# Kernel tuning notes

Measured on AMD Instinct MI355X. Metric: run time of the kernel, lower is better.

The kernel has to match this reference:

```python
import jax, jax.numpy as jnp
import numpy as np


def setup_inputs() -> dict:
    key = jax.random.key(0)
    ks = jax.random.split(key, 10)
    B, C, D, H, W = 2, 512, 8, 32, 32
    Ck = C // 4  # shared KV head dim (and fixed query dim per intended MQA math)
    s = 0.02
    return {
        "x": jax.random.normal(ks[0], (B, C, D, H, W), dtype=jnp.float32),
        "Wq": jax.random.normal(ks[1], (Ck, C), dtype=jnp.float32) * s,
        "bq": jnp.zeros((Ck,), dtype=jnp.float32),
        "Wk": jax.random.normal(ks[2], (Ck, C), dtype=jnp.float32) * s,
        "bk": jnp.zeros((Ck,), dtype=jnp.float32),
        "Wv": jax.random.normal(ks[3], (Ck, C), dtype=jnp.float32) * s,
        "bv": jnp.zeros((Ck,), dtype=jnp.float32),
        "Wo": jax.random.normal(ks[4], (C, C), dtype=jnp.float32) * s,
        "bo": jnp.zeros((C,), dtype=jnp.float32),
    }


def reference(x, Wq, bq, Wk, bk, Wv, bv, Wo, bo):
    B, C, D, H, W = x.shape
    N = D * H * W
    Ck = Wk.shape[0]  # C // 4
    xf = x.reshape(B, C, N)  # flatten spatial dims -> sequence axis
    # 1x1 Conv3d == per-voxel linear projection over channels
    q = jnp.einsum('oc,bcn->bno', Wq, xf) + bq  # [B, N, Ck]
    k = jnp.einsum('oc,bcn->bno', Wk, xf) + bk  # [B, N, Ck]
    v = jnp.einsum('oc,bcn->bno', Wv, xf) + bv  # [B, N, Ck]
    scale = jnp.asarray(Ck, x.dtype) ** -0.5
    attn = jax.nn.softmax(jnp.einsum('bnc,bmc->bnm', q, k) * scale, axis=-1)  # [B, N, N]
    out = jnp.einsum('bnm,bmc->bnc', attn, v)  # [B, N, Ck]
    out = jnp.tile(out, (1, 1, 4))  # repeat(1,1,4) -> [B, N, C]
    out = jnp.einsum('oc,bnc->bon', Wo, out) + bo[None, :, None]  # [B, C, N]
    return out.reshape(B, C, D, H, W) + x
```

## Files before the change

### kernel.cpp

```cpp
#include <hip/hip_runtime.h>
#include <hip/hip_bf16.h>

typedef __bf16 bf16;
typedef __bf16 bf16x8 __attribute__((ext_vector_type(8)));
typedef __bf16 bf16x4 __attribute__((ext_vector_type(4)));
typedef float  f32x4  __attribute__((ext_vector_type(4)));
typedef float  f32x16 __attribute__((ext_vector_type(16)));
typedef unsigned int u32;
typedef u32 u32x4 __attribute__((ext_vector_type(4)));

constexpr int BB = 2, C = 512, NN = 8192, CK = 128;

__device__ __forceinline__ u32 cvt_pk_bf16(float lo, float hi) {
    u32 r;
    asm("v_cvt_pk_bf16_f32 %0, %1, %2" : "=v"(r) : "v"(lo), "v"(hi));
    return r;
}
__device__ __forceinline__ void pl32_swap(u32& a, u32& b) {
    asm("v_permlane32_swap_b32 %0, %1" : "+v"(a), "+v"(b));
}

__global__ __launch_bounds__(256) void k_qkv(
    const float* __restrict__ x,
    const float* __restrict__ Wq, const float* __restrict__ bq,
    const float* __restrict__ Wk, const float* __restrict__ bk,
    const float* __restrict__ Wv, const float* __restrict__ bv,
    bf16* __restrict__ qkv_ws)
{
    const int t = threadIdx.x;
    const int lane = t & 63, w = t >> 6;
    const int lr = lane & 15, lg = lane >> 4;
    const int n0 = blockIdx.x * 128;
    const int which = blockIdx.y;
    const int b = blockIdx.z;
    const float* W    = which == 0 ? Wq : (which == 1 ? Wk : Wv);
    const float* bias = which == 0 ? bq : (which == 1 ? bk : bv);
    bf16* out = qkv_ws + (size_t)which * BB * NN * CK;

    __shared__ __align__(16) char s_xT[128 * 144];
    __shared__ __align__(16) char s_w [128 * 144];

    f32x4 acc[2][8];
#pragma unroll
    for (int m = 0; m < 2; m++)
#pragma unroll
        for (int j = 0; j < 8; j++) acc[m][j] = (f32x4){0.f, 0.f, 0.f, 0.f};

    const float* xb = x + (size_t)b * C * NN;

    const int tok4 = (t & 31) * 4;
    const int c8   = (t >> 5) * 8;
    const int ob   = t >> 2;
    const int c16  = (t & 3) * 16;

    for (int kt = 0; kt < C; kt += 64) {
        __syncthreads();
        {
            float4 v[8];
#pragma unroll
            for (int i = 0; i < 8; i++)
                v[i] = *(const float4*)(xb + (size_t)(kt + c8 + i) * NN + n0 + tok4);
#pragma unroll
            for (int j = 0; j < 4; j++) {
                int tok = tok4 + j;
                bf16x8 pk = { (bf16)v[0].x, (bf16)v[1].x, (bf16)v[2].x, (bf16)v[3].x,
                              (bf16)v[4].x, (bf16)v[5].x, (bf16)v[6].x, (bf16)v[7].x };
                if (j == 1) pk = (bf16x8){ (bf16)v[0].y, (bf16)v[1].y, (bf16)v[2].y, (bf16)v[3].y,
                                           (bf16)v[4].y, (bf16)v[5].y, (bf16)v[6].y, (bf16)v[7].y };
                if (j == 2) pk = (bf16x8){ (bf16)v[0].z, (bf16)v[1].z, (bf16)v[2].z, (bf16)v[3].z,
                                           (bf16)v[4].z, (bf16)v[5].z, (bf16)v[6].z, (bf16)v[7].z };
                if (j == 3) pk = (bf16x8){ (bf16)v[0].w, (bf16)v[1].w, (bf16)v[2].w, (bf16)v[3].w,
                                           (bf16)v[4].w, (bf16)v[5].w, (bf16)v[6].w, (bf16)v[7].w };
                int off = tok * 144 + ((c8 * 2) ^ ((((tok >> 2) & 7)) << 4));
                *(bf16x8*)(s_xT + off) = pk;
            }
        }
#pragma unroll
        for (int p = 0; p < 2; p++) {
            int o = ob + p * 64;
            const float* wp = W + (size_t)o * C + kt + c16;
            float4 a0 = *(const float4*)(wp);
            float4 a1 = *(const float4*)(wp + 4);
            float4 a2 = *(const float4*)(wp + 8);
            float4 a3 = *(const float4*)(wp + 12);
            bf16x8 p0 = { (bf16)a0.x, (bf16)a0.y, (bf16)a0.z, (bf16)a0.w,
                          (bf16)a1.x, (bf16)a1.y, (bf16)a1.z, (bf16)a1.w };
            bf16x8 p1 = { (bf16)a2.x, (bf16)a2.y, (bf16)a2.z, (bf16)a2.w,
                          (bf16)a3.x, (bf16)a3.y, (bf16)a3.z, (bf16)a3.w };
            int perm = ((o >> 2) & 7) << 4;
            *(bf16x8*)(s_w + o * 144 + ((c16 * 2) ^ perm)) = p0;
            *(bf16x8*)(s_w + o * 144 + ((c16 * 2 + 16) ^ perm)) = p1;
        }
        __syncthreads();
#pragma unroll
        for (int ks = 0; ks < 2; ks++) {
            bf16x8 af[2];
#pragma unroll
            for (int m = 0; m < 2; m++) {
                int row = w * 32 + m * 16 + lr;
                af[m] = *(const bf16x8*)(s_xT + row * 144 + ((ks * 64 + lg * 16) ^ ((((row >> 2) & 7)) << 4)));
            }
#pragma unroll
            for (int j = 0; j < 8; j++) {
                int row = j * 16 + lr;
                bf16x8 bfr = *(const bf16x8*)(s_w + row * 144 + ((ks * 64 + lg * 16) ^ ((((row >> 2) & 7)) << 4)));
                acc[0][j] = __builtin_amdgcn_mfma_f32_16x16x32_bf16(af[0], bfr, acc[0][j], 0, 0, 0);
                acc[1][j] = __builtin_amdgcn_mfma_f32_16x16x32_bf16(af[1], bfr, acc[1][j], 0, 0, 0);
            }
        }
    }
#pragma unroll
    for (int m = 0; m < 2; m++)
#pragma unroll
        for (int j = 0; j < 8; j++) {
            int o = j * 16 + lr;
            float bia = bias[o];
#pragma unroll
            for (int r = 0; r < 4; r++) {
                int tok = n0 + w * 32 + m * 16 + lg * 4 + r;
                out[((size_t)b * NN + tok) * CK + o] = (bf16)(acc[m][j][r] + bia);
            }
        }
}

__global__ __launch_bounds__(512, 2) void k_attn(
    const bf16* __restrict__ qkv_ws,
    float* __restrict__ Opart, float* __restrict__ Mw, float* __restrict__ Lw,
    int nsplit)
{
    const int t = threadIdx.x;
    const int lane = t & 63, w = t >> 6;
    const int lq = lane & 31, hi = lane >> 5;

    const int total = 32 * BB * nsplit;
    const int chunkv = total >> 3;
    const int lin = blockIdx.x;
    const int rid = (lin & 7) * chunkv + (lin >> 3);
    const int qt = rid & 31;
    const int bs = rid >> 5;
    const int b = bs & 1, split = bs >> 1;

    const int q0 = qt * 256;
    const int kbeg = split * (NN / nsplit);
    const int nt = (NN / nsplit) / 64;

    const bf16* kg = qkv_ws + (size_t)BB * NN * CK;
    const bf16* vg = qkv_ws + (size_t)2 * BB * NN * CK;

    __shared__ __align__(16) char s_k[2][64 * 256];
    __shared__ __align__(16) char s_vt[2][128 * 128];

    const int kb0 = lq * 256 + ((((lq & 7) ^ hi)) << 4);
    int vbs[4];
#pragma unroll
    for (int db = 0; db < 4; db++) {
        int d = db * 32 + lq;
        vbs[db] = d * 128 + (((((d ^ (d >> 3)) & 7) ^ hi)) << 4);
    }
    const int t2 = t & 255;
    const int sc = t2 & 15, sr = t2 >> 4;
    const int kw_base = (sr * 256 + sc * 16) ^ ((sr & 7) << 4);
    const int vw_base = (sc * 1024 + sr * 8) ^ ((sc & 7) << 4);

    bf16x8 qf[8];
    {
        const float qs = 0.08838834764831845f * 1.4426950408889634f;
        const bf16* qp = qkv_ws + ((size_t)b * NN + q0 + w * 32 + lq) * CK + hi * 8;
#pragma unroll
        for (int ks = 0; ks < 8; ks++) {
            bf16x8 v = *(const bf16x8*)(qp + ks * 16);
#pragma unroll
            for (int i = 0; i < 8; i++) qf[ks][i] = (bf16)((float)v[i] * qs);
        }
    }

    f32x16 oacc[4];
#pragma unroll
    for (int db = 0; db < 4; db++)
#pragma unroll
        for (int i = 0; i < 16; i++) oacc[db][i] = 0.f;
    float mrun = 0.f, lrun = 0.f;

    const bf16* kp = kg + ((size_t)b * NN + kbeg + sr) * CK + sc * 8;
    const bf16* vp = vg + ((size_t)b * NN + kbeg + sr * 4) * CK + sc * 8;
    bf16x8 stg[4];

    auto issue_loads = [&]() {
        if (w < 4) {
#pragma unroll
            for (int p = 0; p < 4; p++) stg[p] = *(const bf16x8*)(kp + (size_t)(16 * p) * CK);
        } else {
#pragma unroll
            for (int p = 0; p < 4; p++) stg[p] = *(const bf16x8*)(vp + (size_t)p * CK);
        }
        kp += (size_t)64 * CK;
        vp += (size_t)64 * CK;
    };

    issue_loads();

    for (int it = 0; it < nt; it++) {
        const int buf = it & 1;
        if (w < 4) {
            char* skw = s_k[buf] + kw_base;
#pragma unroll
            for (int p = 0; p < 4; p++)
                *(bf16x8*)(skw + p * 4096) = stg[p];
        } else {
            char* svw = s_vt[buf];
#pragma unroll
            for (int i = 0; i < 8; i++) {
                bf16x4 pk = { stg[0][i], stg[1][i], stg[2][i], stg[3][i] };
                *(bf16x4*)(svw + (vw_base ^ (i * 144))) = pk;
            }
        }
        __syncthreads();
        if (it + 1 < nt) issue_loads();

        const char* sk = s_k[buf];
        const char* sv = s_vt[buf];

        f32x16 sa0, sa1;
#pragma unroll
        for (int i = 0; i < 16; i++) { sa0[i] = 0.f; sa1[i] = 0.f; }
        __builtin_amdgcn_s_setprio(1);
#pragma unroll
        for (int ks = 0; ks < 8; ks++) {
            bf16x8 kf0 = *(const bf16x8*)(sk + (kb0 ^ (ks * 32)));
            bf16x8 kf1 = *(const bf16x8*)(sk + ((kb0 ^ (ks * 32)) + 8192));
            sa0 = __builtin_amdgcn_mfma_f32_32x32x16_bf16(kf0, qf[ks], sa0, 0, 0, 0);
            sa1 = __builtin_amdgcn_mfma_f32_32x32x16_bf16(kf1, qf[ks], sa1, 0, 0, 0);
        }
        __builtin_amdgcn_s_setprio(0);

        float m8[8];
#pragma unroll
        for (int i = 0; i < 8; i++) m8[i] = fmaxf(sa0[i], sa0[i + 8]);
#pragma unroll
        for (int i = 0; i < 8; i++) m8[i] = fmaxf(m8[i], fmaxf(sa1[i], sa1[i + 8]));
        float pmax = fmaxf(fmaxf(fmaxf(m8[0], m8[1]), fmaxf(m8[2], m8[3])),
                           fmaxf(fmaxf(m8[4], m8[5]), fmaxf(m8[6], m8[7])));
        pmax = fmaxf(pmax, __shfl_xor(pmax, 32));
        bool ok = (pmax <= mrun + 8.f);
        if (!__all(ok)) {
            float mnew = fmaxf(mrun, pmax);
            float corr = exp2f(mrun - mnew);
            mrun = mnew;
            lrun *= corr;
#pragma unroll
            for (int r = 0; r < 16; r++) {
                int qrow = (r & 3) + 8 * (r >> 2) + 4 * hi;
                float co = __shfl(corr, qrow);
#pragma unroll
                for (int db = 0; db < 4; db++) oacc[db][r] *= co;
            }
        }

        f32x16 p0, p1;
#pragma unroll
        for (int i = 0; i < 16; i++) { p0[i] = exp2f(sa0[i] - mrun); p1[i] = exp2f(sa1[i] - mrun); }
        {
            float s0 = ((p0[0] + p0[1]) + (p0[2] + p0[3])) + ((p0[4] + p0[5]) + (p0[6] + p0[7]));
            float s1 = ((p0[8] + p0[9]) + (p0[10] + p0[11])) + ((p0[12] + p0[13]) + (p0[14] + p0[15]));
            float s2 = ((p1[0] + p1[1]) + (p1[2] + p1[3])) + ((p1[4] + p1[5]) + (p1[6] + p1[7]));
            float s3 = ((p1[8] + p1[9]) + (p1[10] + p1[11])) + ((p1[12] + p1[13]) + (p1[14] + p1[15]));
            lrun += (s0 + s1) + (s2 + s3);
        }
        u32 W0[8], W1[8];
#pragma unroll
        for (int j = 0; j < 8; j++) {
            W0[j] = cvt_pk_bf16(p0[2 * j], p0[2 * j + 1]);
            W1[j] = cvt_pk_bf16(p1[2 * j], p1[2 * j + 1]);
        }
        pl32_swap(W0[0], W0[2]); pl32_swap(W0[1], W0[3]);
        pl32_swap(W0[4], W0[6]); pl32_swap(W0[5], W0[7]);
        pl32_swap(W1[0], W1[2]); pl32_swap(W1[1], W1[3]);
        pl32_swap(W1[4], W1[6]); pl32_swap(W1[5], W1[7]);

        __builtin_amdgcn_s_setprio(1);
#pragma unroll
        for (int s = 0; s < 4; s++) {
            u32x4 fw;
            if (s == 0)      fw = (u32x4){W0[0], W0[1], W0[2], W0[3]};
            else if (s == 1) fw = (u32x4){W0[4], W0[5], W0[6], W0[7]};
            else if (s == 2) fw = (u32x4){W1[0], W1[1], W1[2], W1[3]};
            else             fw = (u32x4){W1[4], W1[5], W1[6], W1[7]};
            bf16x8 pa = __builtin_bit_cast(bf16x8, fw);
            const int coff = (s >> 1) * 64 + (s & 1) * 32;
#pragma unroll
            for (int db = 0; db < 4; db++) {
                bf16x8 vf = *(const bf16x8*)(sv + (vbs[db] ^ coff));
                oacc[db] = __builtin_amdgcn_mfma_f32_32x32x16_bf16(pa, vf, oacc[db], 0, 0, 0);
            }
        }
        __builtin_amdgcn_s_setprio(0);
    }

    size_t obase = (((size_t)split * BB + b) * NN + q0 + w * 32);
    float ls = lrun + __shfl_xor(lrun, 32);
    if (lane < 32) {
        Mw[obase + lq] = mrun;
        Lw[obase + lq] = ls;
    }
#pragma unroll
    for (int r = 0; r < 16; r++) {
        int qrow = (r & 3) + 8 * (r >> 2) + 4 * hi;
        float* op = Opart + (obase + qrow) * CK + lq;
#pragma unroll
        for (int db = 0; db < 4; db++) op[db * 32] = oacc[db][r];
    }
}

__global__ __launch_bounds__(256) void k_combine(
    const float* __restrict__ Opart, const float* __restrict__ Mw,
    const float* __restrict__ Lw, bf16* __restrict__ ao, int nsplit)
{
    const int t = threadIdx.x;
    const int b = blockIdx.y;
    const int r0 = blockIdx.x * 64;
    const int d4 = (t & 31) * 4;
#pragma unroll
    for (int p = 0; p < 8; p++) {
        int row = r0 + (t >> 5) + p * 8;
        size_t rbase = (size_t)b * NN + row;
        float M = -1e30f;
        for (int s = 0; s < nsplit; s++)
            M = fmaxf(M, Mw[((size_t)s * BB) * NN + rbase]);
        float L = 0.f;
        float4 acc = {0.f, 0.f, 0.f, 0.f};
        for (int s = 0; s < nsplit; s++) {
            size_t sb = ((size_t)s * BB) * NN + rbase;
            float wgt = exp2f(Mw[sb] - M);
            L += Lw[sb] * wgt;
            float4 v = *(const float4*)(Opart + sb * CK + d4);
            acc.x += v.x * wgt; acc.y += v.y * wgt;
            acc.z += v.z * wgt; acc.w += v.w * wgt;
        }
        float inv = 1.f / L;
        bf16x4 o4 = { (bf16)(acc.x * inv), (bf16)(acc.y * inv),
                      (bf16)(acc.z * inv), (bf16)(acc.w * inv) };
        *(bf16x4*)(ao + rbase * CK + d4) = o4;
    }
}

__global__ __launch_bounds__(256) void k_out(
    const float* __restrict__ x, const float* __restrict__ Wo, const float* __restrict__ bo,
    const bf16* __restrict__ ao, float* __restrict__ y)
{
    const int t = threadIdx.x;
    const int lane = t & 63, w = t >> 6;
    const int lr = lane & 15, lg = lane >> 4;
    const int n0 = blockIdx.x * 128;
    const int o0 = blockIdx.y * 64;
    const int b = blockIdx.z;

    __shared__ __align__(16) char s_w[64 * 256];
    __shared__ __align__(16) char s_a[128 * 256];

    {
        int c4 = (t & 31) * 4, rbase = t >> 5;
#pragma unroll
        for (int p = 0; p < 8; p++) {
            int row = rbase + p * 8;
            const float* wp = Wo + (size_t)(o0 + row) * C + c4;
            float4 a0 = *(const float4*)(wp);
            float4 a1 = *(const float4*)(wp + 128);
            float4 a2 = *(const float4*)(wp + 256);
            float4 a3 = *(const float4*)(wp + 384);
            bf16x4 r4 = { (bf16)(a0.x + a1.x + a2.x + a3.x), (bf16)(a0.y + a1.y + a2.y + a3.y),
                          (bf16)(a0.z + a1.z + a2.z + a3.z), (bf16)(a0.w + a1.w + a2.w + a3.w) };
            int off = (row * 256 + c4 * 2) ^ ((row & 7) << 4);
            *(bf16x4*)(s_w + off) = r4;
        }
    }
    {
        int chunk = t & 15, rbase = t >> 4;
#pragma unroll
        for (int p = 0; p < 8; p++) {
            int row = rbase + p * 16;
            bf16x8 v = *(const bf16x8*)(ao + ((size_t)b * NN + n0 + row) * CK + chunk * 8);
            int off = (row * 256 + chunk * 16) ^ ((row & 7) << 4);
            *(bf16x8*)(s_a + off) = v;
        }
    }
    __syncthreads();

    f32x4 acc[8];
#pragma unroll
    for (int j = 0; j < 8; j++) acc[j] = (f32x4){0.f, 0.f, 0.f, 0.f};
#pragma unroll
    for (int ks = 0; ks < 4; ks++) {
        int row = w * 16 + lr;
        int aoff = (row * 256 + (ks * 32 + lg * 8) * 2) ^ ((row & 7) << 4);
        bf16x8 wf = *(const bf16x8*)(s_w + aoff);
#pragma unroll
        for (int j = 0; j < 8; j++) {
            int nrow = j * 16 + lr;
            int boff = (nrow * 256 + (ks * 32 + lg * 8) * 2) ^ ((nrow & 7) << 4);
            bf16x8 af = *(const bf16x8*)(s_a + boff);
            acc[j] = __builtin_amdgcn_mfma_f32_16x16x32_bf16(wf, af, acc[j], 0, 0, 0);
        }
    }
#pragma unroll
    for (int j = 0; j < 8; j++) {
        int n = n0 + j * 16 + lr;
#pragma unroll
        for (int r = 0; r < 4; r++) {
            int o = o0 + w * 16 + lg * 4 + r;
            size_t idx = ((size_t)b * C + o) * NN + n;
            y[idx] = acc[j][r] + bo[o] + x[idx];
        }
    }
}

extern "C" void kernel_launch(void* const* d_in, const int* in_sizes, int n_in,
                              void* d_out, int out_size, void* d_ws, size_t ws_size,
                              hipStream_t stream)
{
    const float* x  = (const float*)d_in[0];
    const float* Wq = (const float*)d_in[1];
    const float* bq = (const float*)d_in[2];
    const float* Wk = (const float*)d_in[3];
    const float* bk = (const float*)d_in[4];
    const float* Wv = (const float*)d_in[5];
    const float* bv = (const float*)d_in[6];
    const float* Wo = (const float*)d_in[7];
    const float* bo = (const float*)d_in[8];
    float* y = (float*)d_out;

    const size_t qkv_elems = (size_t)3 * BB * NN * CK;
    const size_t ao_elems  = (size_t)BB * NN * CK;

    bf16* qkv = (bf16*)d_ws;
    bf16* ao  = qkv + qkv_elems;
    float* Opart = (float*)(ao + ao_elems);

    int nsplit = 4;
    {
        size_t fixed = (qkv_elems + ao_elems) * sizeof(bf16);
        size_t per_split = ((size_t)BB * NN * CK + 2 * (size_t)BB * NN) * sizeof(float);
        while (nsplit > 1 && fixed + (size_t)nsplit * per_split > ws_size) nsplit >>= 1;
    }
    float* Mw = Opart + (size_t)nsplit * BB * NN * CK;
    float* Lw = Mw + (size_t)nsplit * BB * NN;

    k_qkv<<<dim3(NN / 128, 3, BB), 256, 0, stream>>>(x, Wq, bq, Wk, bk, Wv, bv, qkv);
    k_attn<<<dim3(32 * BB * nsplit, 1, 1), 512, 0, stream>>>(qkv, Opart, Mw, Lw, nsplit);
    k_combine<<<dim3(NN / 64, BB), 256, 0, stream>>>(Opart, Mw, Lw, ao, nsplit);
    k_out<<<dim3(NN / 128, C / 64, BB), 256, 0, stream>>>(x, Wo, bo, ao, y);
}
```

Measured before the change: 155.4 us.

## Process two query tiles per wave in attention to reuse K/V fragments

The attention kernel now uses 256 threads per block, and each wave handles 64 query rows as two 32-row halves that share every K and V fragment read from LDS. This halves LDS fragment reads per MFMA. The score tile is also processed in two 32-key halves, each with its own online-softmax update. Every thread now loads both K and V staging data, which roughly doubles register pressure (two accumulator sets and two Q fragment sets), and launch bounds drop to one block per CU, lowering occupancy.

```diff
diff --git a/kernel.cpp b/kernel.cpp
--- a/kernel.cpp
+++ b/kernel.cpp
@@ -123,7 +123,7 @@
         }
 }
 
-__global__ __launch_bounds__(512, 2) void k_attn(
+__global__ __launch_bounds__(256, 1) void k_attn(
     const bf16* __restrict__ qkv_ws,
     float* __restrict__ Opart, float* __restrict__ Mw, float* __restrict__ Lw,
     int nsplit)
@@ -157,157 +157,196 @@
         int d = db * 32 + lq;
         vbs[db] = d * 128 + (((((d ^ (d >> 3)) & 7) ^ hi)) << 4);
     }
-    const int t2 = t & 255;
-    const int sc = t2 & 15, sr = t2 >> 4;
+    const int sc = t & 15, sr = t >> 4;
     const int kw_base = (sr * 256 + sc * 16) ^ ((sr & 7) << 4);
     const int vw_base = (sc * 1024 + sr * 8) ^ ((sc & 7) << 4);
 
-    bf16x8 qf[8];
+    bf16x8 qfA[8], qfB[8];
     {
         const float qs = 0.08838834764831845f * 1.4426950408889634f;
-        const bf16* qp = qkv_ws + ((size_t)b * NN + q0 + w * 32 + lq) * CK + hi * 8;
+        const bf16* qpA = qkv_ws + ((size_t)b * NN + q0 + w * 64 + lq) * CK + hi * 8;
+        const bf16* qpB = qpA + (size_t)32 * CK;
 #pragma unroll
         for (int ks = 0; ks < 8; ks++) {
-            bf16x8 v = *(const bf16x8*)(qp + ks * 16);
-#pragma unroll
-            for (int i = 0; i < 8; i++) qf[ks][i] = (bf16)((float)v[i] * qs);
-        }
-    }
-
-    f32x16 oacc[4];
+            bf16x8 vA = *(const bf16x8*)(qpA + ks * 16);
+            bf16x8 vB = *(const bf16x8*)(qpB + ks * 16);
+#pragma unroll
+            for (int i = 0; i < 8; i++) {
+                qfA[ks][i] = (bf16)((float)vA[i] * qs);
+                qfB[ks][i] = (bf16)((float)vB[i] * qs);
+            }
+        }
+    }
+
+    f32x16 oaccA[4], oaccB[4];
 #pragma unroll
     for (int db = 0; db < 4; db++)
 #pragma unroll
-        for (int i = 0; i < 16; i++) oacc[db][i] = 0.f;
-    float mrun = 0.f, lrun = 0.f;
+        for (int i = 0; i < 16; i++) { oaccA[db][i] = 0.f; oaccB[db][i] = 0.f; }
+    float mrunA = 0.f, lrunA = 0.f, mrunB = 0.f, lrunB = 0.f;
 
     const bf16* kp = kg + ((size_t)b * NN + kbeg + sr) * CK + sc * 8;
     const bf16* vp = vg + ((size_t)b * NN + kbeg + sr * 4) * CK + sc * 8;
-    bf16x8 stg[4];
+    bf16x8 stgK[4], stgV[4];
 
     auto issue_loads = [&]() {
-        if (w < 4) {
-#pragma unroll
-            for (int p = 0; p < 4; p++) stg[p] = *(const bf16x8*)(kp + (size_t)(16 * p) * CK);
-        } else {
-#pragma unroll
-            for (int p = 0; p < 4; p++) stg[p] = *(const bf16x8*)(vp + (size_t)p * CK);
-        }
+#pragma unroll
+        for (int p = 0; p < 4; p++) stgK[p] = *(const bf16x8*)(kp + (size_t)(16 * p) * CK);
+#pragma unroll
+        for (int p = 0; p < 4; p++) stgV[p] = *(const bf16x8*)(vp + (size_t)p * CK);
         kp += (size_t)64 * CK;
         vp += (size_t)64 * CK;
     };
 
-    issue_loads();
-
-    for (int it = 0; it < nt; it++) {
-        const int buf = it & 1;
-        if (w < 4) {
-            char* skw = s_k[buf] + kw_base;
-#pragma unroll
-            for (int p = 0; p < 4; p++)
-                *(bf16x8*)(skw + p * 4096) = stg[p];
-        } else {
-            char* svw = s_vt[buf];
-#pragma unroll
-            for (int i = 0; i < 8; i++) {
-                bf16x4 pk = { stg[0][i], stg[1][i], stg[2][i], stg[3][i] };
-                *(bf16x4*)(svw + (vw_base ^ (i * 144))) = pk;
-            }
-        }
-        __syncthreads();
-        if (it + 1 < nt) issue_loads();
-
-        const char* sk = s_k[buf];
-        const char* sv = s_vt[buf];
-
-        f32x16 sa0, sa1;
-#pragma unroll
-        for (int i = 0; i < 16; i++) { sa0[i] = 0.f; sa1[i] = 0.f; }
-        __builtin_amdgcn_s_setprio(1);
-#pragma unroll
-        for (int ks = 0; ks < 8; ks++) {
-            bf16x8 kf0 = *(const bf16x8*)(sk + (kb0 ^ (ks * 32)));
-            bf16x8 kf1 = *(const bf16x8*)(sk + ((kb0 ^ (ks * 32)) + 8192));
-            sa0 = __builtin_amdgcn_mfma_f32_32x32x16_bf16(kf0, qf[ks], sa0, 0, 0, 0);
-            sa1 = __builtin_amdgcn_mfma_f32_32x32x16_bf16(kf1, qf[ks], sa1, 0, 0, 0);
-        }
-        __builtin_amdgcn_s_setprio(0);
-
-        float m8[8];
-#pragma unroll
-        for (int i = 0; i < 8; i++) m8[i] = fmaxf(sa0[i], sa0[i + 8]);
-#pragma unroll
-        for (int i = 0; i < 8; i++) m8[i] = fmaxf(m8[i], fmaxf(sa1[i], sa1[i + 8]));
-        float pmax = fmaxf(fmaxf(fmaxf(m8[0], m8[1]), fmaxf(m8[2], m8[3])),
-                           fmaxf(fmaxf(m8[4], m8[5]), fmaxf(m8[6], m8[7])));
+    auto softmax_half = [&](f32x16& sa, float& mrun, float& lrun, float& oscale) {
+        float a0 = fmaxf(fmaxf(sa[0], sa[1]), sa[2]);
+        float a1 = fmaxf(fmaxf(sa[3], sa[4]), sa[5]);
+        float a2 = fmaxf(fmaxf(sa[6], sa[7]), sa[8]);
+        float a3 = fmaxf(fmaxf(sa[9], sa[10]), sa[11]);
+        float a4 = fmaxf(fmaxf(sa[12], sa[13]), sa[14]);
+        float pmax = fmaxf(fmaxf(fmaxf(a0, a1), fmaxf(a2, a3)), fmaxf(a4, sa[15]));
         pmax = fmaxf(pmax, __shfl_xor(pmax, 32));
-        bool ok = (pmax <= mrun + 8.f);
-        if (!__all(ok)) {
+        oscale = 1.f;
+        if (!__all(pmax <= mrun + 8.f)) {
             float mnew = fmaxf(mrun, pmax);
             float corr = exp2f(mrun - mnew);
             mrun = mnew;
             lrun *= corr;
-#pragma unroll
-            for (int r = 0; r < 16; r++) {
-                int qrow = (r & 3) + 8 * (r >> 2) + 4 * hi;
-                float co = __shfl(corr, qrow);
-#pragma unroll
-                for (int db = 0; db < 4; db++) oacc[db][r] *= co;
-            }
-        }
-
-        f32x16 p0, p1;
-#pragma unroll
-        for (int i = 0; i < 16; i++) { p0[i] = exp2f(sa0[i] - mrun); p1[i] = exp2f(sa1[i] - mrun); }
+            oscale = corr;
+        }
+    };
+
+    issue_loads();
+
+    for (int it = 0; it < nt; it++) {
+        const int buf = it & 1;
         {
-            float s0 = ((p0[0] + p0[1]) + (p0[2] + p0[3])) + ((p0[4] + p0[5]) + (p0[6] + p0[7]));
-            float s1 = ((p0[8] + p0[9]) + (p0[10] + p0[11])) + ((p0[12] + p0[13]) + (p0[14] + p0[15]));
-            float s2 = ((p1[0] + p1[1]) + (p1[2] + p1[3])) + ((p1[4] + p1[5]) + (p1[6] + p1[7]));
-            float s3 = ((p1[8] + p1[9]) + (p1[10] + p1[11])) + ((p1[12] + p1[13]) + (p1[14] + p1[15]));
-            lrun += (s0 + s1) + (s2 + s3);
-        }
-        u32 W0[8], W1[8];
-#pragma unroll
-        for (int j = 0; j < 8; j++) {
-            W0[j] = cvt_pk_bf16(p0[2 * j], p0[2 * j + 1]);
-            W1[j] = cvt_pk_bf16(p1[2 * j], p1[2 * j + 1]);
-        }
-        pl32_swap(W0[0], W0[2]); pl32_swap(W0[1], W0[3]);
-        pl32_swap(W0[4], W0[6]); pl32_swap(W0[5], W0[7]);
-        pl32_swap(W1[0], W1[2]); pl32_swap(W1[1], W1[3]);
-        pl32_swap(W1[4], W1[6]); pl32_swap(W1[5], W1[7]);
-
-        __builtin_amdgcn_s_setprio(1);
-#pragma unroll
-        for (int s = 0; s < 4; s++) {
-            u32x4 fw;
-            if (s == 0)      fw = (u32x4){W0[0], W0[1], W0[2], W0[3]};
-            else if (s == 1) fw = (u32x4){W0[4], W0[5], W0[6], W0[7]};
-            else if (s == 2) fw = (u32x4){W1[0], W1[1], W1[2], W1[3]};
-            else             fw = (u32x4){W1[4], W1[5], W1[6], W1[7]};
-            bf16x8 pa = __builtin_bit_cast(bf16x8, fw);
-            const int coff = (s >> 1) * 64 + (s & 1) * 32;
-#pragma unroll
-            for (int db = 0; db < 4; db++) {
-                bf16x8 vf = *(const bf16x8*)(sv + (vbs[db] ^ coff));
-                oacc[db] = __builtin_amdgcn_mfma_f32_32x32x16_bf16(pa, vf, oacc[db], 0, 0, 0);
-            }
-        }
-        __builtin_amdgcn_s_setprio(0);
-    }
-
-    size_t obase = (((size_t)split * BB + b) * NN + q0 + w * 32);
-    float ls = lrun + __shfl_xor(lrun, 32);
-    if (lane < 32) {
-        Mw[obase + lq] = mrun;
-        Lw[obase + lq] = ls;
-    }
-#pragma unroll
-    for (int r = 0; r < 16; r++) {
-        int qrow = (r & 3) + 8 * (r >> 2) + 4 * hi;
-        float* op = Opart + (obase + qrow) * CK + lq;
-#pragma unroll
-        for (int db = 0; db < 4; db++) op[db * 32] = oacc[db][r];
+            char* skw = s_k[buf] + kw_base;
+#pragma unroll
+            for (int p = 0; p < 4; p++)
+                *(bf16x8*)(skw + p * 4096) = stgK[p];
+            char* svw = s_vt[buf];
+#pragma unroll
+            for (int i = 0; i < 8; i++) {
+                bf16x4 pk = { stgV[0][i], stgV[1][i], stgV[2][i], stgV[3][i] };
+                *(bf16x4*)(svw + (vw_base ^ (i * 144))) = pk;
+            }
+        }
+        __syncthreads();
+        if (it + 1 < nt) issue_loads();
+
+        const char* sk = s_k[buf];
+        const char* sv = s_vt[buf];
+
+#pragma unroll
+        for (int h = 0; h < 2; h++) {
+            f32x16 saA, saB;
+#pragma unroll
+            for (int i = 0; i < 16; i++) { saA[i] = 0.f; saB[i] = 0.f; }
+            __builtin_amdgcn_s_setprio(1);
+#pragma unroll
+            for (int ks = 0; ks < 8; ks++) {
+                bf16x8 kf = *(const bf16x8*)(sk + ((kb0 ^ (ks * 32)) + h * 8192));
+                saA = __builtin_amdgcn_mfma_f32_32x32x16_bf16(kf, qfA[ks], saA, 0, 0, 0);
+                saB = __builtin_amdgcn_mfma_f32_32x32x16_bf16(kf, qfB[ks], saB, 0, 0, 0);
+            }
+            __builtin_amdgcn_s_setprio(0);
+
+            float osA, osB;
+            softmax_half(saA, mrunA, lrunA, osA);
+            softmax_half(saB, mrunB, lrunB, osB);
+            if (osA != 1.f) {
+#pragma unroll
+                for (int r = 0; r < 16; r++) {
+                    int qrow = (r & 3) + 8 * (r >> 2) + 4 * hi;
+                    float co = __shfl(osA, qrow);
+#pragma unroll
+                    for (int db = 0; db < 4; db++) oaccA[db][r] *= co;
+                }
+            }
+            if (osB != 1.f) {
+#pragma unroll
+                for (int r = 0; r < 16; r++) {
+                    int qrow = (r & 3) + 8 * (r >> 2) + 4 * hi;
+                    float co = __shfl(osB, qrow);
+#pragma unroll
+                    for (int db = 0; db < 4; db++) oaccB[db][r] *= co;
+                }
+            }
+
+            u32 WA[8], WB[8];
+            {
+                f32x16 pA, pB;
+#pragma unroll
+                for (int i = 0; i < 16; i++) {
+                    pA[i] = exp2f(saA[i] - mrunA);
+                    pB[i] = exp2f(saB[i] - mrunB);
+                }
+                float sA = (((pA[0] + pA[1]) + (pA[2] + pA[3])) + ((pA[4] + pA[5]) + (pA[6] + pA[7])))
+                         + (((pA[8] + pA[9]) + (pA[10] + pA[11])) + ((pA[12] + pA[13]) + (pA[14] + pA[15])));
+                float sB = (((pB[0] + pB[1]) + (pB[2] + pB[3])) + ((pB[4] + pB[5]) + (pB[6] + pB[7])))
+                         + (((pB[8] + pB[9]) + (pB[10] + pB[11])) + ((pB[12] + pB[13]) + (pB[14] + pB[15])));
+                lrunA += sA;
+                lrunB += sB;
+#pragma unroll
+                for (int j = 0; j < 8; j++) {
+                    WA[j] = cvt_pk_bf16(pA[2 * j], pA[2 * j + 1]);
+                    WB[j] = cvt_pk_bf16(pB[2 * j], pB[2 * j + 1]);
+                }
+            }
+            pl32_swap(WA[0], WA[2]); pl32_swap(WA[1], WA[3]);
+            pl32_swap(WA[4], WA[6]); pl32_swap(WA[5], WA[7]);
+            pl32_swap(WB[0], WB[2]); pl32_swap(WB[1], WB[3]);
+            pl32_swap(WB[4], WB[6]); pl32_swap(WB[5], WB[7]);
+
+            __builtin_amdgcn_s_setprio(1);
+#pragma unroll
+            for (int s2 = 0; s2 < 2; s2++) {
+                u32x4 fwA = s2 == 0 ? (u32x4){WA[0], WA[1], WA[2], WA[3]}
+                                    : (u32x4){WA[4], WA[5], WA[6], WA[7]};
+                u32x4 fwB = s2 == 0 ? (u32x4){WB[0], WB[1], WB[2], WB[3]}
+                                    : (u32x4){WB[4], WB[5], WB[6], WB[7]};
+                bf16x8 paA = __builtin_bit_cast(bf16x8, fwA);
+                bf16x8 paB = __builtin_bit_cast(bf16x8, fwB);
+                const int coff = h * 64 + s2 * 32;
+#pragma unroll
+                for (int db = 0; db < 4; db++) {
+                    bf16x8 vf = *(const bf16x8*)(sv + (vbs[db] ^ coff));
+                    oaccA[db] = __builtin_amdgcn_mfma_f32_32x32x16_bf16(paA, vf, oaccA[db], 0, 0, 0);
+                    oaccB[db] = __builtin_amdgcn_mfma_f32_32x32x16_bf16(paB, vf, oaccB[db], 0, 0, 0);
+                }
+            }
+            __builtin_amdgcn_s_setprio(0);
+        }
+    }
+
+    {
+        size_t obase = (((size_t)split * BB + b) * NN + q0 + w * 64);
+        float ls = lrunA + __shfl_xor(lrunA, 32);
+        if (lane < 32) {
+            Mw[obase + lq] = mrunA;
+            Lw[obase + lq] = ls;
+        }
+#pragma unroll
+        for (int r = 0; r < 16; r++) {
+            int qrow = (r & 3) + 8 * (r >> 2) + 4 * hi;
+            float* op = Opart + (obase + qrow) * CK + lq;
+#pragma unroll
+            for (int db = 0; db < 4; db++) op[db * 32] = oaccA[db][r];
+        }
+        obase += 32;
+        ls = lrunB + __shfl_xor(lrunB, 32);
+        if (lane < 32) {
+            Mw[obase + lq] = mrunB;
+            Lw[obase + lq] = ls;
+        }
+#pragma unroll
+        for (int r = 0; r < 16; r++) {
+            int qrow = (r & 3) + 8 * (r >> 2) + 4 * hi;
+            float* op = Opart + (obase + qrow) * CK + lq;
+#pragma unroll
+            for (int db = 0; db < 4; db++) op[db * 32] = oaccB[db][r];
+        }
     }
 }
 
@@ -445,7 +484,7 @@
     float* Lw = Mw + (size_t)nsplit * BB * NN;
 
     k_qkv<<<dim3(NN / 128, 3, BB), 256, 0, stream>>>(x, Wq, bq, Wk, bk, Wv, bv, qkv);
-    k_attn<<<dim3(32 * BB * nsplit, 1, 1), 512, 0, stream>>>(qkv, Opart, Mw, Lw, nsplit);
+    k_attn<<<dim3(32 * BB * nsplit, 1, 1), 256, 0, stream>>>(qkv, Opart, Mw, Lw, nsplit);
     k_combine<<<dim3(NN / 64, BB), 256, 0, stream>>>(Opart, Mw, Lw, ao, nsplit);
     k_out<<<dim3(NN / 128, C / 64, BB), 256, 0, stream>>>(x, Wo, bo, ao, y);
 }
```

Result: slower. 203.7 us (+31.0%).
